# Kernel optimization log

Measured on AMD Instinct MI355X. Metric: run time of the kernel, lower is better.

The kernel has to match this reference:

```python
import jax, jax.numpy as jnp
import numpy as np

B, S, E = 4, 2048, 2048
H = 16
DH = 2048 // H  # head dim = 128


def setup_inputs() -> dict:
    key = jax.random.key(0)
    k0, k1, k2, k3 = jax.random.split(key, 4)
    scale = 1.0 / np.sqrt(E)
    embedded = jax.random.normal(k0, (B, S, E), dtype=jnp.float32)
    # stacked per-head projection weights, bias-free Linear: y = x @ W^T -> store as [H, E, DH]
    Wq = jax.random.normal(k1, (H, E, DH), dtype=jnp.float32) * scale
    Wk = jax.random.normal(k2, (H, E, DH), dtype=jnp.float32) * scale
    Wv = jax.random.normal(k3, (H, E, DH), dtype=jnp.float32) * scale
    return {"embedded": embedded, "Wq": Wq, "Wk": Wk, "Wv": Wv}


def reference(embedded, Wq, Wk, Wv):
    # batched over heads instead of the original python loop (same math)
    q = jnp.einsum("bse,hed->bhsd", embedded, Wq)
    k = jnp.einsum("bse,hed->bhsd", embedded, Wk)
    v = jnp.einsum("bse,hed->bhsd", embedded, Wv)
    scores = jnp.einsum("bhsd,bhtd->bhst", q, k) / jnp.sqrt(jnp.float32(DH))
    causal = jnp.tril(jnp.ones((S, S), dtype=bool))  # [S, S]
    scores = jnp.where(causal, scores, -jnp.inf)
    probs = jax.nn.softmax(scores, axis=-1)
    out = jnp.einsum("bhst,bhtd->bhsd", probs, v)
    cated = out.transpose(0, 2, 1, 3).reshape(B, S, H * DH)  # concat heads on dim=2
    return jnp.round(cated, 4)
```

## Files before the change

kernel.cpp:

```cpp
#include <hip/hip_runtime.h>

typedef float   f32x4 __attribute__((ext_vector_type(4)));
typedef _Float16 half8 __attribute__((ext_vector_type(8)));
typedef _Float16 half4 __attribute__((ext_vector_type(4)));

#define B_  4
#define S_  2048
#define E_  2048
#define H_  16
#define DH_ 128

__device__ __forceinline__ void gld16(const void* g, void* l) {
  __builtin_amdgcn_global_load_lds((const void __attribute__((address_space(1)))*)g,
                                   (void __attribute__((address_space(3)))*)l, 16, 0, 0);
}

__global__ __launch_bounds__(256) void k_cvt(const float* __restrict__ in,
                                             _Float16* __restrict__ out) {
  size_t i = ((size_t)blockIdx.x * 256 + threadIdx.x) * 8;
  float4 a = *(const float4*)(in + i);
  float4 b = *(const float4*)(in + i + 4);
  half8 h;
  h[0]=(_Float16)a.x; h[1]=(_Float16)a.y; h[2]=(_Float16)a.z; h[3]=(_Float16)a.w;
  h[4]=(_Float16)b.x; h[5]=(_Float16)b.y; h[6]=(_Float16)b.z; h[7]=(_Float16)b.w;
  *(half8*)(out + i) = h;
}

__global__ __launch_bounds__(256) void k_wt(const float* __restrict__ Wq, const float* __restrict__ Wk,
                                            const float* __restrict__ Wv, _Float16* __restrict__ Wqt,
                                            _Float16* __restrict__ Wkt, _Float16* __restrict__ Wvt) {
  __shared__ float t[32][33];
  int p = blockIdx.z >> 4, h = blockIdx.z & 15;
  const float* W  = (p==0) ? Wq  : (p==1) ? Wk  : Wv;
  _Float16*    Wt = (p==0) ? Wqt : (p==1) ? Wkt : Wvt;
  int e0 = blockIdx.x * 32, d0 = blockIdx.y * 32;
  int tx = threadIdx.x, ty = threadIdx.y;
  for (int i=0;i<4;i++)
    t[ty+8*i][tx] = W[((size_t)h*E_ + (e0+ty+8*i))*DH_ + d0+tx];
  __syncthreads();
  for (int i=0;i<4;i++)
    Wt[((size_t)h*DH_ + (d0+ty+8*i))*E_ + e0+tx] = (_Float16)t[tx][ty+8*i];
}

#define NT 32

__global__ __launch_bounds__(512, 2) void k_gemm(const _Float16* __restrict__ X,
    const _Float16* __restrict__ Wq, const _Float16* __restrict__ Wk, const _Float16* __restrict__ Wv,
    _Float16* __restrict__ Qo, _Float16* __restrict__ Ko, _Float16* __restrict__ Vt)
{
  __shared__ __align__(16) _Float16 pool[65536];

  const int z = blockIdx.z;
  const _Float16* Wp = (z==0) ? Wq : (z==1) ? Wk : Wv;

  const int fi  = blockIdx.x + (blockIdx.y << 5);
  const int lbx = fi >> 3, lby = fi & 7;
  const int m0 = lbx << 8, n0 = lby << 8;

  const int tid = threadIdx.x;
  const int wid = tid >> 6, lane = tid & 63, quad = lane >> 4, lcol = lane & 15;
  const int wm = wid >> 2, wn = wid & 3;

  int soff[2]; int slds[2];
  #pragma unroll
  for (int r=0;r<2;r++){
    int chunk = wid*128 + r*64 + lane;
    int row = chunk >> 3, cl = chunk & 7, cg = cl ^ (row & 7);
    soff[r] = row*E_ + cg*8;
    slds[r] = (wid*128 + r*64) * 16;
  }

  const _Float16* Ag = X  + (size_t)m0 * E_;
  const _Float16* Bg = Wp + (size_t)n0 * E_;

  auto stageA = [&](int mh, int tt, int buf){
    const _Float16* s = Ag + mh*(128*E_) + tt*64;
    char* l = (char*)pool + (buf*4096 + mh*1024)*16;
    #pragma unroll
    for (int r=0;r<2;r++) gld16(s + soff[r], l + slds[r]);
  };
  auto stageB = [&](int nh, int tt, int buf){
    const _Float16* s = Bg + nh*(128*E_) + tt*64;
    char* l = (char*)pool + (buf*4096 + (2+nh)*1024)*16;
    #pragma unroll
    for (int r=0;r<2;r++) gld16(s + soff[r], l + slds[r]);
  };

  half8 a[2][4], b[2][2];
  f32x4 acc[2][2][4][2] = {};

  auto rdA = [&](int mh, int buf){
    const _Float16* base = pool + (buf*4096 + mh*1024)*8;
    #pragma unroll
    for (int kk=0;kk<2;kk++)
      #pragma unroll
      for (int mi=0;mi<4;mi++){
        int R = wm*64 + mi*16 + lcol;
        int c = (kk*4 + quad) ^ (R & 7);
        a[kk][mi] = *(const half8*)(base + R*64 + c*8);
      }
  };
  auto rdB = [&](int nh, int buf){
    const _Float16* base = pool + (buf*4096 + (2+nh)*1024)*8;
    #pragma unroll
    for (int kk=0;kk<2;kk++)
      #pragma unroll
      for (int ni=0;ni<2;ni++){
        int R = wn*32 + ni*16 + lcol;
        int c = (kk*4 + quad) ^ (R & 7);
        b[kk][ni] = *(const half8*)(base + R*64 + c*8);
      }
  };
  auto mm = [&](f32x4 (&ac)[4][2]){
    #pragma unroll
    for (int kk=0;kk<2;kk++)
      #pragma unroll
      for (int mi=0;mi<4;mi++)
        #pragma unroll
        for (int ni=0;ni<2;ni++)
          ac[mi][ni] = __builtin_amdgcn_mfma_f32_16x16x32_f16(a[kk][mi], b[kk][ni], ac[mi][ni], 0, 0, 0);
  };

  stageA(0,0,0); stageB(0,0,0); stageA(1,0,0); stageB(1,0,0);
  stageA(0,1,1); stageB(1,1,1); stageA(1,1,1);
  asm volatile("s_waitcnt vmcnt(6)" ::: "memory");
  __builtin_amdgcn_s_barrier();

#define MFMA_OPEN() do{ __builtin_amdgcn_s_barrier(); \
    asm volatile("s_waitcnt lgkmcnt(0)" ::: "memory"); \
    __builtin_amdgcn_sched_barrier(0); \
    __builtin_amdgcn_s_setprio(1); }while(0)
#define MFMA_CLOSE() do{ __builtin_amdgcn_s_setprio(0); \
    __builtin_amdgcn_s_barrier(); }while(0)

#define TILE(T, BUF) do{ \
    rdA(0, BUF); rdB(0, BUF); \
    if ((T)+1 < NT) stageB(0, (T)+1, (BUF)^1); \
    MFMA_OPEN(); mm(acc[0][0]); MFMA_CLOSE(); \
    rdB(1, BUF); \
    if ((T)+2 < NT) stageA(0, (T)+2, BUF); \
    MFMA_OPEN(); mm(acc[0][1]); MFMA_CLOSE(); \
    rdA(1, BUF); \
    if ((T)+2 < NT) stageB(1, (T)+2, BUF); \
    MFMA_OPEN(); mm(acc[1][1]); MFMA_CLOSE(); \
    rdB(0, BUF); \
    if ((T)+2 < NT) stageA(1, (T)+2, BUF); \
    __builtin_amdgcn_s_barrier(); \
    asm volatile("s_waitcnt lgkmcnt(0)" ::: "memory"); \
    __builtin_amdgcn_sched_barrier(0); \
    __builtin_amdgcn_s_setprio(1); \
    mm(acc[1][0]); \
    __builtin_amdgcn_s_setprio(0); \
    if ((T) < NT-2)       { asm volatile("s_waitcnt vmcnt(6)" ::: "memory"); } \
    else if ((T) == NT-2) { asm volatile("s_waitcnt vmcnt(0)" ::: "memory"); } \
    __builtin_amdgcn_s_barrier(); \
  }while(0)

  for (int t = 0; t < NT; t += 2){
    TILE(t,   0);
    TILE(t+1, 1);
  }
#undef TILE
#undef MFMA_OPEN
#undef MFMA_CLOSE

  const int bb = m0 >> 11;
  const int s0 = m0 & 2047;
  const int h0 = n0 >> 7;
  if (z < 2){
    _Float16* O = z ? Ko : Qo;
    #pragma unroll
    for (int mh=0; mh<2; mh++)
      #pragma unroll
      for (int nh=0; nh<2; nh++)
        #pragma unroll
        for (int mi=0; mi<4; mi++)
          #pragma unroll
          for (int ni=0; ni<2; ni++){
            const int srow = s0 + mh*128 + wm*64 + mi*16 + quad*4;
            const int d = wn*32 + ni*16 + lcol;
            _Float16* p = O + (((size_t)bb*H_ + (h0+nh))*S_ + srow)*DH_ + d;
            const f32x4 v = acc[mh][nh][mi][ni];
            p[0]=(_Float16)v[0]; p[DH_]=(_Float16)v[1]; p[2*DH_]=(_Float16)v[2]; p[3*DH_]=(_Float16)v[3];
          }
  } else {
    #pragma unroll
    for (int mh=0; mh<2; mh++)
      #pragma unroll
      for (int nh=0; nh<2; nh++)
        #pragma unroll
        for (int mi=0; mi<4; mi++)
          #pragma unroll
          for (int ni=0; ni<2; ni++){
            const int scol = s0 + mh*128 + wm*64 + mi*16 + quad*4;
            const int d = wn*32 + ni*16 + lcol;
            const f32x4 u = acc[mh][nh][mi][ni];
            half4 v;
            v[0]=(_Float16)u[0]; v[1]=(_Float16)u[1]; v[2]=(_Float16)u[2]; v[3]=(_Float16)u[3];
            *(half4*)(Vt + (((size_t)bb*H_ + (h0+nh))*DH_ + d)*S_ + scol) = v;
          }
  }
}

__global__ __launch_bounds__(512) void k_attn(const _Float16* __restrict__ Q,
    const _Float16* __restrict__ K, const _Float16* __restrict__ Vt, float* __restrict__ out)
{
  __shared__ __align__(16) _Float16 Ks[2][8192], Vs[2][8192];

  const int b = blockIdx.z, h = blockIdx.y;
  const int q0 = (gridDim.x - 1 - blockIdx.x) * 128;
  const int tid = threadIdx.x, wid = tid >> 6, lane = tid & 63, quad = lane >> 4, lcol = lane & 15;
  const size_t bh = (size_t)b*H_ + h;
  const _Float16* Qg = Q  + (bh*S_ + q0)*DH_;
  const _Float16* Kg = K  + bh*S_*DH_;
  const _Float16* Vg = Vt + bh*DH_*S_;

  int krow[2], kcg[2], vdr[2], vcg[2];
  for (int r=0;r<2;r++){
    int chunk = wid*128 + r*64 + lane;
    krow[r] = chunk >> 4;
    kcg[r]  = (chunk & 15) ^ (krow[r] & 15);
    vdr[r]  = chunk >> 3;
    vcg[r]  = (chunk & 7) ^ (vdr[r] & 7);
  }

  half8 qf[4];
  for (int kk=0; kk<4; kk++)
    qf[kk] = *(const half8*)(Qg + (size_t)(wid*16 + lcol)*DH_ + kk*32 + quad*8);

  for (int r=0;r<2;r++){
    gld16(Kg + (size_t)krow[r]*DH_ + kcg[r]*8, (char*)Ks[0] + wid*2048 + r*1024 + lane*16);
    gld16(Vg + (size_t)vdr[r]*S_ + 0 + vcg[r]*8, (char*)Vs[0] + wid*2048 + r*1024 + lane*16);
  }

  f32x4 oaccT[8] = {};
  f32x4 lacc = {};
  const half4 ones = {(_Float16)1.f,(_Float16)1.f,(_Float16)1.f,(_Float16)1.f};
  const float c1 = 0.12751879526654326f;
  const float c2 = -11.541560327111707f;
  const int rbase = q0 + wid*16;
  const int nt = (q0 >> 6) + 2;

  for (int t = 0; t < nt; t++) {
    const int buf = t & 1;
    const _Float16* ksb = Ks[buf];
    const _Float16* vsb = Vs[buf];
    const int j0 = t << 6;
    const bool live = (j0 <= rbase + 15);
    __syncthreads();

    f32x4 sa[4] = {};
    if (live){
      for (int kk=0; kk<4; kk++){
        int cl = (kk*4 + quad) ^ lcol;
        for (int jb=0; jb<4; jb++){
          half8 kf = *(const half8*)(ksb + (size_t)(jb*16 + lcol)*DH_ + cl*8);
          sa[jb] = __builtin_amdgcn_mfma_f32_16x16x32_f16(kf, qf[kk], sa[jb], 0, 0, 0);
        }
      }
    }

    if (t+1 < nt){
      const int j1 = (t+1) << 6;
      for (int r=0;r<2;r++){
        gld16(Kg + (size_t)(j1+krow[r])*DH_ + kcg[r]*8, (char*)Ks[buf^1] + wid*2048 + r*1024 + lane*16);
        gld16(Vg + (size_t)vdr[r]*S_ + j1 + vcg[r]*8,   (char*)Vs[buf^1] + wid*2048 + r*1024 + lane*16);
      }
    }

    if (live){
      half4 pb[4];
      if (j0 + 63 > rbase){
        for (int jb=0; jb<4; jb++)
          for (int rg=0; rg<4; rg++){
            int j = jb*16 + quad*4 + rg;
            float p = (j0 + j > rbase + lcol) ? 0.f
                    : __builtin_amdgcn_exp2f(fmaf(sa[jb][rg], c1, c2));
            pb[jb][rg] = (_Float16)p;
          }
      } else {
        for (int jb=0; jb<4; jb++)
          for (int rg=0; rg<4; rg++)
            pb[jb][rg] = (_Float16)__builtin_amdgcn_exp2f(fmaf(sa[jb][rg], c1, c2));
      }

      for (int jb=0; jb<4; jb++)
        lacc = __builtin_amdgcn_mfma_f32_16x16x16f16(ones, pb[jb], lacc, 0, 0, 0);

      for (int dblk=0; dblk<8; dblk++){
        const _Float16* vrow = vsb + (size_t)(dblk*16 + lcol)*64;
        for (int jb=0; jb<4; jb++){
          int cl = (2*jb + (quad>>1)) ^ (lcol & 7);
          half4 va = *(const half4*)(vrow + cl*8 + (quad&1)*4);
          oaccT[dblk] = __builtin_amdgcn_mfma_f32_16x16x16f16(va, pb[jb], oaccT[dblk], 0, 0, 0);
        }
      }
    }
  }

  const float rinv = 1.f / lacc[0];
  const int s = q0 + wid*16 + lcol;
  float* op = out + ((size_t)b*S_ + s)*(H_*DH_) + h*DH_ + quad*4;
  for (int dblk=0; dblk<8; dblk++){
    float4 v;
    v.x = oaccT[dblk][0]*rinv; v.y = oaccT[dblk][1]*rinv;
    v.z = oaccT[dblk][2]*rinv; v.w = oaccT[dblk][3]*rinv;
    *(float4*)(op + dblk*16) = v;
  }
}

extern "C" void kernel_launch(void* const* d_in, const int* in_sizes, int n_in,
                              void* d_out, int out_size, void* d_ws, size_t ws_size,
                              hipStream_t stream) {
  const float* X  = (const float*)d_in[0];
  const float* Wq = (const float*)d_in[1];
  const float* Wk = (const float*)d_in[2];
  const float* Wv = (const float*)d_in[3];
  float* out = (float*)d_out;

  _Float16* Xh  = (_Float16*)d_ws;
  _Float16* Wqt = Xh  + (size_t)B_*S_*E_;
  _Float16* Wkt = Wqt + (size_t)H_*E_*DH_;
  _Float16* Wvt = Wkt + (size_t)H_*E_*DH_;
  _Float16* Qh  = Wvt + (size_t)H_*E_*DH_;
  _Float16* Kh  = Qh  + (size_t)B_*H_*S_*DH_;
  _Float16* Vth = Kh  + (size_t)B_*H_*S_*DH_;

  k_cvt <<<8192, 256, 0, stream>>>(X, Xh);
  k_wt  <<<dim3(E_/32, DH_/32, 3*H_), dim3(32,8), 0, stream>>>(Wq, Wk, Wv, Wqt, Wkt, Wvt);
  k_gemm<<<dim3(32, 8, 3), 512, 0, stream>>>(Xh, Wqt, Wkt, Wvt, Qh, Kh, Vth);
  k_attn<<<dim3(S_/128, H_, B_), 512, 0, stream>>>(Qh, Kh, Vth, out);
}
```

Before: 532.2 us.

## Process 256 query rows per attention block, two 16-row groups per wave

Each wave now handles two 16-row query groups, so each K/V tile staged in LDS and each K/V fragment read from LDS feeds twice as many MFMAs. The block's query tile grows from 128 to 256 rows, halving the grid and the K/V global traffic per query. A launch-bounds hint for two blocks per CU is added. In exchange, accumulator register pressure doubles and the grid has fewer blocks, which can leave CUs idle or imbalanced under the causal workload.

Result: faster. 493.5 us (-7.3%).

```diff
diff --git a/kernel.cpp b/kernel.cpp
--- a/kernel.cpp
+++ b/kernel.cpp
@@ -202,13 +202,13 @@
   }
 }
 
-__global__ __launch_bounds__(512) void k_attn(const _Float16* __restrict__ Q,
+__global__ __launch_bounds__(512, 2) void k_attn(const _Float16* __restrict__ Q,
     const _Float16* __restrict__ K, const _Float16* __restrict__ Vt, float* __restrict__ out)
 {
   __shared__ __align__(16) _Float16 Ks[2][8192], Vs[2][8192];
 
   const int b = blockIdx.z, h = blockIdx.y;
-  const int q0 = (gridDim.x - 1 - blockIdx.x) * 128;
+  const int q0 = (gridDim.x - 1 - blockIdx.x) * 256;
   const int tid = threadIdx.x, wid = tid >> 6, lane = tid & 63, quad = lane >> 4, lcol = lane & 15;
   const size_t bh = (size_t)b*H_ + h;
   const _Float16* Qg = Q  + (bh*S_ + q0)*DH_;
@@ -224,38 +224,49 @@
     vcg[r]  = (chunk & 7) ^ (vdr[r] & 7);
   }
 
-  half8 qf[4];
-  for (int kk=0; kk<4; kk++)
-    qf[kk] = *(const half8*)(Qg + (size_t)(wid*16 + lcol)*DH_ + kk*32 + quad*8);
+  half8 qf[2][4];
+  for (int g=0; g<2; g++)
+    for (int kk=0; kk<4; kk++)
+      qf[g][kk] = *(const half8*)(Qg + (size_t)(wid*32 + g*16 + lcol)*DH_ + kk*32 + quad*8);
 
   for (int r=0;r<2;r++){
     gld16(Kg + (size_t)krow[r]*DH_ + kcg[r]*8, (char*)Ks[0] + wid*2048 + r*1024 + lane*16);
     gld16(Vg + (size_t)vdr[r]*S_ + 0 + vcg[r]*8, (char*)Vs[0] + wid*2048 + r*1024 + lane*16);
   }
 
-  f32x4 oaccT[8] = {};
-  f32x4 lacc = {};
+  f32x4 oaccT[2][8] = {};
+  f32x4 lacc[2] = {};
   const half4 ones = {(_Float16)1.f,(_Float16)1.f,(_Float16)1.f,(_Float16)1.f};
   const float c1 = 0.12751879526654326f;
   const float c2 = -11.541560327111707f;
-  const int rbase = q0 + wid*16;
-  const int nt = (q0 >> 6) + 2;
+  const int rbase = q0 + wid*32;
+  const int nt = (q0 >> 6) + 4;
 
   for (int t = 0; t < nt; t++) {
     const int buf = t & 1;
     const _Float16* ksb = Ks[buf];
     const _Float16* vsb = Vs[buf];
     const int j0 = t << 6;
-    const bool live = (j0 <= rbase + 15);
+    const bool live0 = (j0 <= rbase + 15);
+    const bool live1 = (j0 <= rbase + 31);
     __syncthreads();
 
-    f32x4 sa[4] = {};
-    if (live){
+    f32x4 sa[2][4] = {};
+    if (live0){
       for (int kk=0; kk<4; kk++){
         int cl = (kk*4 + quad) ^ lcol;
         for (int jb=0; jb<4; jb++){
           half8 kf = *(const half8*)(ksb + (size_t)(jb*16 + lcol)*DH_ + cl*8);
-          sa[jb] = __builtin_amdgcn_mfma_f32_16x16x32_f16(kf, qf[kk], sa[jb], 0, 0, 0);
+          sa[0][jb] = __builtin_amdgcn_mfma_f32_16x16x32_f16(kf, qf[0][kk], sa[0][jb], 0, 0, 0);
+          sa[1][jb] = __builtin_amdgcn_mfma_f32_16x16x32_f16(kf, qf[1][kk], sa[1][jb], 0, 0, 0);
+        }
+      }
+    } else if (live1){
+      for (int kk=0; kk<4; kk++){
+        int cl = (kk*4 + quad) ^ lcol;
+        for (int jb=0; jb<4; jb++){
+          half8 kf = *(const half8*)(ksb + (size_t)(jb*16 + lcol)*DH_ + cl*8);
+          sa[1][jb] = __builtin_amdgcn_mfma_f32_16x16x32_f16(kf, qf[1][kk], sa[1][jb], 0, 0, 0);
         }
       }
     }
@@ -268,44 +279,66 @@
       }
     }
 
-    if (live){
-      half4 pb[4];
-      if (j0 + 63 > rbase){
+    if (live1){
+      half4 pb[2][4];
+      auto sm = [&](f32x4 (&s4)[4], half4 (&p4)[4], int rb){
+        if (j0 + 63 > rb){
+          for (int jb=0; jb<4; jb++)
+            for (int rg=0; rg<4; rg++){
+              int j = jb*16 + quad*4 + rg;
+              float p = (j0 + j > rb + lcol) ? 0.f
+                      : __builtin_amdgcn_exp2f(fmaf(s4[jb][rg], c1, c2));
+              p4[jb][rg] = (_Float16)p;
+            }
+        } else {
+          for (int jb=0; jb<4; jb++)
+            for (int rg=0; rg<4; rg++)
+              p4[jb][rg] = (_Float16)__builtin_amdgcn_exp2f(fmaf(s4[jb][rg], c1, c2));
+        }
+      };
+
+      if (live0){
+        sm(sa[0], pb[0], rbase);
+        sm(sa[1], pb[1], rbase + 16);
+        for (int jb=0; jb<4; jb++){
+          lacc[0] = __builtin_amdgcn_mfma_f32_16x16x16f16(ones, pb[0][jb], lacc[0], 0, 0, 0);
+          lacc[1] = __builtin_amdgcn_mfma_f32_16x16x16f16(ones, pb[1][jb], lacc[1], 0, 0, 0);
+        }
+        for (int dblk=0; dblk<8; dblk++){
+          const _Float16* vrow = vsb + (size_t)(dblk*16 + lcol)*64;
+          for (int jb=0; jb<4; jb++){
+            int cl = (2*jb + (quad>>1)) ^ (lcol & 7);
+            half4 va = *(const half4*)(vrow + cl*8 + (quad&1)*4);
+            oaccT[0][dblk] = __builtin_amdgcn_mfma_f32_16x16x16f16(va, pb[0][jb], oaccT[0][dblk], 0, 0, 0);
+            oaccT[1][dblk] = __builtin_amdgcn_mfma_f32_16x16x16f16(va, pb[1][jb], oaccT[1][dblk], 0, 0, 0);
+          }
+        }
+      } else {
+        sm(sa[1], pb[1], rbase + 16);
         for (int jb=0; jb<4; jb++)
-          for (int rg=0; rg<4; rg++){
-            int j = jb*16 + quad*4 + rg;
-            float p = (j0 + j > rbase + lcol) ? 0.f
-                    : __builtin_amdgcn_exp2f(fmaf(sa[jb][rg], c1, c2));
-            pb[jb][rg] = (_Float16)p;
+          lacc[1] = __builtin_amdgcn_mfma_f32_16x16x16f16(ones, pb[1][jb], lacc[1], 0, 0, 0);
+        for (int dblk=0; dblk<8; dblk++){
+          const _Float16* vrow = vsb + (size_t)(dblk*16 + lcol)*64;
+          for (int jb=0; jb<4; jb++){
+            int cl = (2*jb + (quad>>1)) ^ (lcol & 7);
+            half4 va = *(const half4*)(vrow + cl*8 + (quad&1)*4);
+            oaccT[1][dblk] = __builtin_amdgcn_mfma_f32_16x16x16f16(va, pb[1][jb], oaccT[1][dblk], 0, 0, 0);
           }
-      } else {
-        for (int jb=0; jb<4; jb++)
-          for (int rg=0; rg<4; rg++)
-            pb[jb][rg] = (_Float16)__builtin_amdgcn_exp2f(fmaf(sa[jb][rg], c1, c2));
-      }
-
-      for (int jb=0; jb<4; jb++)
-        lacc = __builtin_amdgcn_mfma_f32_16x16x16f16(ones, pb[jb], lacc, 0, 0, 0);
-
-      for (int dblk=0; dblk<8; dblk++){
-        const _Float16* vrow = vsb + (size_t)(dblk*16 + lcol)*64;
-        for (int jb=0; jb<4; jb++){
-          int cl = (2*jb + (quad>>1)) ^ (lcol & 7);
-          half4 va = *(const half4*)(vrow + cl*8 + (quad&1)*4);
-          oaccT[dblk] = __builtin_amdgcn_mfma_f32_16x16x16f16(va, pb[jb], oaccT[dblk], 0, 0, 0);
         }
       }
     }
   }
 
-  const float rinv = 1.f / lacc[0];
-  const int s = q0 + wid*16 + lcol;
-  float* op = out + ((size_t)b*S_ + s)*(H_*DH_) + h*DH_ + quad*4;
-  for (int dblk=0; dblk<8; dblk++){
-    float4 v;
-    v.x = oaccT[dblk][0]*rinv; v.y = oaccT[dblk][1]*rinv;
-    v.z = oaccT[dblk][2]*rinv; v.w = oaccT[dblk][3]*rinv;
-    *(float4*)(op + dblk*16) = v;
+  for (int g=0; g<2; g++){
+    const float rinv = 1.f / lacc[g][0];
+    const int s = q0 + wid*32 + g*16 + lcol;
+    float* op = out + ((size_t)b*S_ + s)*(H_*DH_) + h*DH_ + quad*4;
+    for (int dblk=0; dblk<8; dblk++){
+      float4 v;
+      v.x = oaccT[g][dblk][0]*rinv; v.y = oaccT[g][dblk][1]*rinv;
+      v.z = oaccT[g][dblk][2]*rinv; v.w = oaccT[g][dblk][3]*rinv;
+      *(float4*)(op + dblk*16) = v;
+    }
   }
 }
 
@@ -329,5 +362,5 @@
   k_cvt <<<8192, 256, 0, stream>>>(X, Xh);
   k_wt  <<<dim3(E_/32, DH_/32, 3*H_), dim3(32,8), 0, stream>>>(Wq, Wk, Wv, Wqt, Wkt, Wvt);
   k_gemm<<<dim3(32, 8, 3), 512, 0, stream>>>(Xh, Wqt, Wkt, Wvt, Qh, Kh, Vth);
-  k_attn<<<dim3(S_/128, H_, B_), 512, 0, stream>>>(Qh, Kh, Vth, out);
-}
+  k_attn<<<dim3(S_/256, H_, B_), 512, 0, stream>>>(Qh, Kh, Vth, out);
+}
```
